# Optimization experiments

Hardware: AMD Instinct MI355X
Metric: run time of the kernel (lower is better)

Reference implementation:

```python
import jax, jax.numpy as jnp
import numpy as np

CLS_THR = 0.7      # cls_threshold
NMS_THR = 0.7      # nms_threshold
MAX_OUT = 100      # nms_max_outputs
MIN_SIZE = 3.0     # min_size_threshold


def setup_inputs() -> dict:
    key = jax.random.key(0)
    k1, k2 = jax.random.split(key)
    B, H, W, A = 1, 128, 128, 9
    img_h = img_w = 2048
    # build valid pixel-space boxes [y1,x1,y2,x2] with y2>y1, x2>x1
    r = jax.random.uniform(k1, (B, H, W, A, 4), dtype=jnp.float32)
    y1 = r[..., 0] * (img_h - 200.0)
    x1 = r[..., 1] * (img_w - 200.0)
    y2 = y1 + 1.0 + r[..., 2] * 199.0
    x2 = x1 + 1.0 + r[..., 3] * 199.0
    proposals = jnp.stack([y1, x1, y2, x2], axis=-1).reshape(B, H, W, A * 4)
    cls_score = jax.random.normal(k2, (B, H, W, A * 2), dtype=jnp.float32) * 2.0
    return {"proposals": proposals, "cls_score": cls_score,
            "image_h": img_h, "image_w": img_w}


def reference(proposals, cls_score, image_h, image_w):
    B, H, W = proposals.shape[0], proposals.shape[1], proposals.shape[2]
    A = proposals.shape[3] // 4
    boxes = proposals.reshape(-1, 4)                       # [N,4] yxyx, pixels
    prob = jax.nn.softmax(cls_score.reshape(B, H, W, A, 2), axis=-1)
    score0 = prob[..., 0].reshape(-1)                      # [N] objectness
    # threshold mask (tf boolean_mask replaced by fixed-shape invalidation)
    active0 = jnp.where(score0 > CLS_THR, score0, -1.0)
    areas = (boxes[:, 2] - boxes[:, 0]) * (boxes[:, 3] - boxes[:, 1])

    def nms_step(active, _):
        idx = jnp.argmax(active)
        ok = active[idx] > 0.0                             # any box left?
        b = boxes[idx]
        yy1 = jnp.maximum(b[0], boxes[:, 0])
        xx1 = jnp.maximum(b[1], boxes[:, 1])
        yy2 = jnp.minimum(b[2], boxes[:, 2])
        xx2 = jnp.minimum(b[3], boxes[:, 3])
        inter = jnp.maximum(yy2 - yy1, 0.0) * jnp.maximum(xx2 - xx1, 0.0)
        iou = inter / (areas + areas[idx] - inter + 1e-9)
        active = jnp.where(iou > NMS_THR, -1.0, active)
        active = active.at[idx].set(-1.0)
        return active, (idx, ok)

    _, (idxs, oks) = jax.lax.scan(nms_step, active0, None, length=MAX_OUT)
    sel_boxes = boxes[idxs]                                # [100,4]
    sel_cls = score0[idxs]                                 # [100]
    # remove_small_proposals: h,w from yxyx -> yxhw
    hgt = sel_boxes[:, 2] - sel_boxes[:, 0]
    wid = sel_boxes[:, 3] - sel_boxes[:, 1]
    keep = oks & (hgt > MIN_SIZE) & (wid > MIN_SIZE)
    sel_boxes = jnp.where(keep[:, None], sel_boxes, 0.0)
    sel_cls = jnp.where(keep, sel_cls, 0.0)
    # format == 'percentage': exact pixel coords -> fraction of image
    scale = jnp.array([image_h, image_w, image_h, image_w], dtype=jnp.float32)
    sel_boxes = (sel_boxes / scale)[None]                  # [1,100,4]
    return sel_boxes, sel_cls[None]                        # [1,100]
```

## Files before the change

kernel.cpp:

```cpp
#include <hip/hip_runtime.h>


#define CLS_THR 0.7f
#define NMS_THR 0.7f
#define MAX_OUT 100
#define MIN_SZ  3.0f

#define N_CAP      147456
#define BASE_BITS  0x3F333334u
#define BIN_SHIFT  9
#define NBINS      9831
#define HIST_WORDS 10240
#define PAD_WORD   10000
#define CTR_WORD   10100
#define TARGET     160u
#define CAP        512
#define CHUNK      128
#define BUCKET_NB  1024
#define BUCKET_LO  (NBINS - BUCKET_NB)
#define BCAP       64

__device__ __forceinline__ float softmax0(float l0, float l1) {
    float m  = fmaxf(l0, l1);
    float e0 = expf(l0 - m);
    float e1 = expf(l1 - m);
    return e0 / (e0 + e1);
}

__device__ __forceinline__ unsigned int ld_dev_u32(const unsigned int* p) {
    return __hip_atomic_load(p, __ATOMIC_RELAXED, __HIP_MEMORY_SCOPE_AGENT);
}
__device__ __forceinline__ unsigned long long ld_dev_u64(const unsigned long long* p) {
    return __hip_atomic_load(p, __ATOMIC_RELAXED, __HIP_MEMORY_SCOPE_AGENT);
}
__device__ __forceinline__ void st_dev_u64(unsigned long long* p, unsigned long long v) {
    __hip_atomic_store(p, v, __ATOMIC_RELAXED, __HIP_MEMORY_SCOPE_AGENT);
}

__launch_bounds__(256)
__global__ void fused_kernel(const float4* __restrict__ boxes,
                             const float4* __restrict__ cls,
                             unsigned int* hist,
                             unsigned long long* bucket,
                             const int* __restrict__ ph, const int* __restrict__ pw,
                             float* __restrict__ out, int N, int nblocks)
{
    __shared__ unsigned long long s_kbuf[CAP];
    __shared__ unsigned long long s_sorted[CAP];
    __shared__ float4 s_bbox[CAP];
    __shared__ unsigned int s_sup[CHUNK][4];
    __shared__ unsigned int s_rowflag[4];
    __shared__ unsigned int s_seedm[4];
    __shared__ unsigned int s_keep[4];
    __shared__ unsigned int s_gpack[CAP];
    __shared__ unsigned int s_goff[CAP];
    __shared__ float  s_klist[MAX_OUT][5];
    __shared__ float4 s_kbox[MAX_OUT];
    __shared__ float  s_karea[MAX_OUT];
    __shared__ int s_cbin, s_ov, s_kept, s_ne, s_last;
    __shared__ unsigned int s_M, s_cnt;

    const int tid  = threadIdx.x;
    const int lane = tid & 63;
    const int wave = tid >> 6;

    const unsigned int X = hist[PAD_WORD];

    {
        int t = blockIdx.x * 256 + tid;
        int i = t * 2;
        if (i < N) {
            float4 v = cls[t];
            float p0 = softmax0(v.x, v.y);
            float p1 = (i + 1 < N) ? softmax0(v.z, v.w) : 0.0f;
            if (p0 > CLS_THR) {
                unsigned int b = __float_as_uint(p0);
                int bin = (int)((b - BASE_BITS) >> BIN_SHIFT);
                unsigned int slot = atomicAdd(&hist[bin], 1u) - X;
                if (bin >= BUCKET_LO && slot < BCAP)
                    st_dev_u64(&bucket[(size_t)(bin - BUCKET_LO) * BCAP + slot],
                        ((unsigned long long)b << 32) | (unsigned int)(~i));
            }
            if (p1 > CLS_THR) {
                unsigned int b = __float_as_uint(p1);
                int bin = (int)((b - BASE_BITS) >> BIN_SHIFT);
                unsigned int slot = atomicAdd(&hist[bin], 1u) - X;
                if (bin >= BUCKET_LO && slot < BCAP)
                    st_dev_u64(&bucket[(size_t)(bin - BUCKET_LO) * BCAP + slot],
                        ((unsigned long long)b << 32) | (unsigned int)(~(i + 1)));
            }
        }
    }
    asm volatile("s_waitcnt vmcnt(0)" ::: "memory");
    __syncthreads();
    if (tid == 0) {
        unsigned int old = atomicAdd(&hist[CTR_WORD], 1u);
        s_last = (old - X == (unsigned int)(nblocks - 1)) ? 1 : 0;
    }
    __syncthreads();
    if (!s_last) return;

    const float img_h = (float)(*ph);
    const float img_w = (float)(*pw);

    int kept = 0;
    int hi = NBINS;
    bool done = false;

    while (!done) {
        if (wave == 0) {
            int pos = hi; unsigned int run = 0u; int cb = -1;
            unsigned int M = 0u; int ov = 0;
            while (pos > 0) {
                int b = pos - 1 - lane;
                unsigned int h = (b >= 0) ? (ld_dev_u32(&hist[b]) - X) : 0u;
                unsigned int pref = h;
                #pragma unroll
                for (int o = 1; o < 64; o <<= 1) {
                    unsigned int t2 = __shfl_up(pref, o);
                    if (lane >= o) pref += t2;
                }
                unsigned int cum = run + pref;
                unsigned long long okm = __ballot(b >= 0 && cum >= TARGET);
                unsigned long long ovm = __ballot(b >= 0 && h > BCAP);
                if (okm) {
                    int first = __builtin_ctzll(okm);
                    cb = pos - 1 - first;
                    M  = __shfl(cum, first);
                    unsigned long long lm = (first >= 63) ? ~0ull
                                          : ((1ull << (first + 1)) - 1ull);
                    if (ovm & lm) ov = 1;
                    break;
                }
                if (ovm) ov = 1;
                run += __shfl(pref, 63);
                pos -= 64;
            }
            if (cb < 0) { cb = 0; M = run; }
            if (lane == 0) { s_cbin = cb; s_M = M; s_ov = ov;
                             s_cnt = 0u; s_ne = 0; }
        }
        __syncthreads();
        const int cbin = s_cbin;
        const unsigned int M = s_M;
        if (M == 0u) break;
        const unsigned int M_eff = (M > CAP) ? CAP : M;
        const bool usebucket = (!s_ov) && (cbin >= BUCKET_LO);

        if (usebucket) {
            if (wave == 0) {
                int pos = hi; unsigned int run = 0u; int ne = 0;
                while (pos > cbin) {
                    int b = pos - 1 - lane;
                    unsigned int h = (b >= cbin) ? (ld_dev_u32(&hist[b]) - X) : 0u;
                    unsigned int pref = h;
                    #pragma unroll
                    for (int o = 1; o < 64; o <<= 1) {
                        unsigned int t2 = __shfl_up(pref, o);
                        if (lane >= o) pref += t2;
                    }
                    unsigned int offv = run + pref - h;
                    unsigned long long nzm = __ballot(h > 0u);
                    int slot = ne + __popcll(nzm & ((1ull << lane) - 1ull));
                    if (h > 0u && slot < CAP) {
                        s_gpack[slot] = ((unsigned int)b << 16) | h;
                        s_goff[slot]  = offv;
                    }
                    ne  += __popcll(nzm);
                    run += __shfl(pref, 63);
                    pos -= 64;
                }
                if (lane == 0) s_ne = ne;
            }
            __syncthreads();
            int ne = s_ne; if (ne > CAP) ne = CAP;
            for (int e = wave; e < ne; e += 4) {
                unsigned int pk = s_gpack[e];
                int b = (int)(pk >> 16);
                unsigned int cnt = pk & 0xFFFFu;
                unsigned int off = s_goff[e];
                if (lane < (int)cnt && off + lane < CAP)
                    s_kbuf[off + lane] =
                        ld_dev_u64(&bucket[(size_t)(b - BUCKET_LO) * BCAP + lane]);
            }
        } else {
            unsigned int th_lo = BASE_BITS + ((unsigned int)cbin << BIN_SHIFT);
            unsigned int th_hi = BASE_BITS + ((unsigned int)hi   << BIN_SHIFT);
            int NV = N >> 1;
            for (int basei = 0; basei < NV; basei += 256 * 8) {
                float4 v[8];
                #pragma unroll
                for (int u = 0; u < 8; ++u) {
                    int i4 = basei + u * 256 + tid;
                    v[u] = (i4 < NV) ? cls[i4]
                                     : make_float4(0.f, 0.f, 0.f, 0.f);
                }
                #pragma unroll
                for (int u = 0; u < 8; ++u) {
                    int i0 = (basei + u * 256 + tid) * 2;
                    float p0 = softmax0(v[u].x, v[u].y);
                    float p1 = softmax0(v[u].z, v[u].w);
                    if (p0 > CLS_THR) {
                        unsigned int b = __float_as_uint(p0);
                        if (b >= th_lo && b < th_hi) {
                            unsigned int sl = atomicAdd(&s_cnt, 1u);
                            if (sl < CAP)
                                s_kbuf[sl] = ((unsigned long long)b << 32)
                                           | (unsigned int)(~i0);
                        }
                    }
                    if (p1 > CLS_THR) {
                        unsigned int b = __float_as_uint(p1);
                        if (b >= th_lo && b < th_hi) {
                            unsigned int sl = atomicAdd(&s_cnt, 1u);
                            if (sl < CAP)
                                s_kbuf[sl] = ((unsigned long long)b << 32)
                                           | (unsigned int)(~(i0 + 1));
                        }
                    }
                }
            }
        }
        __syncthreads();

        for (unsigned int t = tid; t < M_eff; t += 256) {
            unsigned long long kt = s_kbuf[t];
            unsigned int rank = 0u;
            #pragma unroll 8
            for (unsigned int j = 0; j < M_eff; ++j)
                rank += (s_kbuf[j] > kt) ? 1u : 0u;
            s_sorted[rank] = kt;
        }
        __syncthreads();

        for (unsigned int t = tid; t < M_eff; t += 256) {
            int idx = (int)(~(unsigned int)s_sorted[t]);
            s_bbox[t] = boxes[idx];
        }
        __syncthreads();

        int base = 0;
        while (base < (int)M_eff && kept < MAX_OUT) {
            int C = (int)M_eff - base; if (C > CHUNK) C = CHUNK;
            if (tid < CHUNK) { s_sup[tid][0] = 0u; s_sup[tid][1] = 0u;
                               s_sup[tid][2] = 0u; s_sup[tid][3] = 0u; }
            if (tid < 4) { s_rowflag[tid] = 0u; s_seedm[tid] = 0u;
                           s_keep[tid] = 0u; }
            __syncthreads();

            if (kept > 0 && (tid & 127) < C) {
                int i = tid & 127;
                float4 cb = s_bbox[base + i];
                float ca = (cb.z - cb.x) * (cb.w - cb.y);
                bool sup = false;
                for (int j = (tid >> 7); j < kept; j += 2) {
                    float4 kb = s_kbox[j];
                    float yy1 = fmaxf(cb.x, kb.x), xx1 = fmaxf(cb.y, kb.y);
                    float yy2 = fminf(cb.z, kb.z), xx2 = fminf(cb.w, kb.w);
                    float it = fmaxf(yy2 - yy1, 0.f) * fmaxf(xx2 - xx1, 0.f);
                    sup = sup ||
                        (it / (ca + s_karea[j] - it + 1e-9f) > NMS_THR);
                }
                if (sup) atomicOr(&s_seedm[i >> 5], 1u << (i & 31));
            }
            for (int d = 1 + wave; d < C; d += 4) {
                #pragma unroll
                for (int half = 0; half < 2; ++half) {
                    int i = lane + half * 64;
                    if (i + d < C) {
                        float4 a  = s_bbox[base + i];
                        float4 b2 = s_bbox[base + i + d];
                        float aa = (a.z - a.x) * (a.w - a.y);
                        float ab = (b2.z - b2.x) * (b2.w - b2.y);
                        float yy1 = fmaxf(a.x, b2.x), xx1 = fmaxf(a.y, b2.y);
                        float yy2 = fminf(a.z, b2.z), xx2 = fminf(a.w, b2.w);
                        float it = fmaxf(yy2 - yy1, 0.f) * fmaxf(xx2 - xx1, 0.f);
                        if (it / (aa + ab - it + 1e-9f) > NMS_THR) {
                            int j = i + d;
                            atomicOr(&s_sup[i][j >> 5], 1u << (j & 31));
                            atomicOr(&s_rowflag[i >> 5], 1u << (i & 31));
                        }
                    }
                }
            }
            __syncthreads();

            if (wave == 0) {
                unsigned int ku[4] = {0u, 0u, 0u, 0u};
                unsigned int mg[4] = {s_seedm[0], s_seedm[1],
                                      s_seedm[2], s_seedm[3]};
                int k = kept;
                #pragma unroll
                for (int g = 0; g < 4; ++g) {
                    int lo = g * 32;
                    if (lo < C && k < MAX_OUT) {
                        int cg = C - lo; if (cg > 32) cg = 32;
                        unsigned int vmask = (cg >= 32) ? 0xFFFFFFFFu
                                            : ((1u << cg) - 1u);
                        unsigned int avail = vmask & ~mg[g];
                        unsigned int hitr = s_rowflag[g] & avail;
                        if (hitr == 0u) {
                            int c2 = __popc(avail);
                            int need = MAX_OUT - k;
                            if (c2 <= need) { ku[g] |= avail; k += c2; }
                            else {
                                unsigned int kw = avail; int cc = c2;
                                while (cc > need) {
                                    kw &= ~(0x80000000u >> __builtin_clz(kw));
                                    --cc;
                                }
                                ku[g] |= kw; k = MAX_OUT;
                            }
                        } else {
                            unsigned int rem = avail;
                            while (rem && k < MAX_OUT) {
                                int b = __builtin_ctz(rem);
                                ku[g] |= (1u << b); ++k;
                                if ((s_rowflag[g] >> b) & 1u) {
                                    int i = lo + b;
                                    mg[0] |= s_sup[i][0];
                                    mg[1] |= s_sup[i][1];
                                    mg[2] |= s_sup[i][2];
                                    mg[3] |= s_sup[i][3];
                                    rem &= ~mg[g];
                                }
                                rem &= ~(1u << b);
                            }
                        }
                    }
                }
                if (lane == 0) {
                    s_keep[0] = ku[0]; s_keep[1] = ku[1];
                    s_keep[2] = ku[2]; s_keep[3] = ku[3];
                    s_kept = k;
                }
            }
            __syncthreads();
            int prevkept = kept;
            kept = s_kept;

            if (tid < C) {
                int w = tid >> 5, bp = tid & 31;
                unsigned int kw = s_keep[w];
                if ((kw >> bp) & 1u) {
                    int pre = __popc(kw & ((1u << bp) - 1u));
                    for (int q = 0; q < w; ++q) pre += __popc(s_keep[q]);
                    int slot = prevkept + pre;
                    float4 bb = s_bbox[base + tid];
                    s_klist[slot][0] = bb.x; s_klist[slot][1] = bb.y;
                    s_klist[slot][2] = bb.z; s_klist[slot][3] = bb.w;
                    s_klist[slot][4] = __uint_as_float(
                        (unsigned int)(s_sorted[base + tid] >> 32));
                    s_kbox[slot]  = bb;
                    s_karea[slot] = (bb.z - bb.x) * (bb.w - bb.y);
                }
            }
            __syncthreads();
            base += C;
        }

        done = (kept >= MAX_OUT) || (cbin == 0);
        hi = cbin;
    }

    __syncthreads();
    for (int j = tid; j < 4 * MAX_OUT + MAX_OUT; j += 256) {
        float val = 0.0f;
        if (j < 4 * MAX_OUT) {
            int k = j >> 2, cc = j & 3;
            if (k < kept) {
                float h = s_klist[k][2] - s_klist[k][0];
                float w = s_klist[k][3] - s_klist[k][1];
                if (h > MIN_SZ && w > MIN_SZ) {
                    float scale = (cc == 0 || cc == 2) ? img_h : img_w;
                    val = s_klist[k][cc] / scale;
                }
            }
        } else {
            int k = j - 4 * MAX_OUT;
            if (k < kept) {
                float h = s_klist[k][2] - s_klist[k][0];
                float w = s_klist[k][3] - s_klist[k][1];
                if (h > MIN_SZ && w > MIN_SZ) val = s_klist[k][4];
            }
        }
        out[j] = val;
    }
}

extern "C" void kernel_launch(void* const* d_in, const int* in_sizes, int n_in,
                              void* d_out, int out_size, void* d_ws, size_t ws_size,
                              hipStream_t stream) {
    const float* proposals = (const float*)d_in[0];
    const float* cls       = (const float*)d_in[1];
    const int*   ph        = (const int*)d_in[2];
    const int*   pw        = (const int*)d_in[3];
    float*       out       = (float*)d_out;

    int N = in_sizes[0] / 4;
    if (N > N_CAP) N = N_CAP;

    char* ws = (char*)d_ws;
    unsigned long long* bucket = (unsigned long long*)ws;
    unsigned int* hist = (unsigned int*)(ws + (size_t)BUCKET_NB * BCAP * 8);

    int nblocks = (N / 2 + 255) / 256;
    fused_kernel<<<nblocks, 256, 0, stream>>>(
        (const float4*)proposals, (const float4*)cls, hist, bucket,
        ph, pw, out, N, nblocks);
}
```

Baseline: 84.14 us.

## Store box coords in bucket and add 256-thread fast path for candidate selection

```diff
diff --git a/kernel.cpp b/kernel.cpp
--- a/kernel.cpp
+++ b/kernel.cpp
@@ -36,6 +36,9 @@
 __device__ __forceinline__ void st_dev_u64(unsigned long long* p, unsigned long long v) {
     __hip_atomic_store(p, v, __ATOMIC_RELAXED, __HIP_MEMORY_SCOPE_AGENT);
 }
+__device__ __forceinline__ unsigned long long pack2f(float a, float b) {
+    return ((unsigned long long)__float_as_uint(b) << 32) | __float_as_uint(a);
+}
 
 __launch_bounds__(256)
 __global__ void fused_kernel(const float4* __restrict__ boxes,
@@ -48,16 +51,18 @@
     __shared__ unsigned long long s_kbuf[CAP];
     __shared__ unsigned long long s_sorted[CAP];
     __shared__ float4 s_bbox[CAP];
+    __shared__ unsigned int s_binof[CAP];
     __shared__ unsigned int s_sup[CHUNK][4];
     __shared__ unsigned int s_rowflag[4];
     __shared__ unsigned int s_seedm[4];
     __shared__ unsigned int s_keep[4];
     __shared__ unsigned int s_gpack[CAP];
     __shared__ unsigned int s_goff[CAP];
+    __shared__ unsigned int s_wsum[4];
     __shared__ float  s_klist[MAX_OUT][5];
     __shared__ float4 s_kbox[MAX_OUT];
     __shared__ float  s_karea[MAX_OUT];
-    __shared__ int s_cbin, s_ov, s_kept, s_ne, s_last;
+    __shared__ int s_cbin, s_ov, s_kept, s_ne, s_last, s_cutT;
     __shared__ unsigned int s_M, s_cnt;
 
     const int tid  = threadIdx.x;
@@ -70,24 +75,34 @@
         int t = blockIdx.x * 256 + tid;
         int i = t * 2;
         if (i < N) {
-            float4 v = cls[t];
+            float4 v  = cls[t];
+            float4 b0 = boxes[i];
+            float4 b1 = (i + 1 < N) ? boxes[i + 1] : b0;
             float p0 = softmax0(v.x, v.y);
             float p1 = (i + 1 < N) ? softmax0(v.z, v.w) : 0.0f;
             if (p0 > CLS_THR) {
                 unsigned int b = __float_as_uint(p0);
                 int bin = (int)((b - BASE_BITS) >> BIN_SHIFT);
                 unsigned int slot = atomicAdd(&hist[bin], 1u) - X;
-                if (bin >= BUCKET_LO && slot < BCAP)
-                    st_dev_u64(&bucket[(size_t)(bin - BUCKET_LO) * BCAP + slot],
+                if (bin >= BUCKET_LO && slot < BCAP) {
+                    size_t ba = ((size_t)(bin - BUCKET_LO) * BCAP + slot) * 3;
+                    st_dev_u64(&bucket[ba],
                         ((unsigned long long)b << 32) | (unsigned int)(~i));
+                    st_dev_u64(&bucket[ba + 1], pack2f(b0.x, b0.y));
+                    st_dev_u64(&bucket[ba + 2], pack2f(b0.z, b0.w));
+                }
             }
             if (p1 > CLS_THR) {
                 unsigned int b = __float_as_uint(p1);
                 int bin = (int)((b - BASE_BITS) >> BIN_SHIFT);
                 unsigned int slot = atomicAdd(&hist[bin], 1u) - X;
-                if (bin >= BUCKET_LO && slot < BCAP)
-                    st_dev_u64(&bucket[(size_t)(bin - BUCKET_LO) * BCAP + slot],
+                if (bin >= BUCKET_LO && slot < BCAP) {
+                    size_t ba = ((size_t)(bin - BUCKET_LO) * BCAP + slot) * 3;
+                    st_dev_u64(&bucket[ba],
                         ((unsigned long long)b << 32) | (unsigned int)(~(i + 1)));
+                    st_dev_u64(&bucket[ba + 1], pack2f(b1.x, b1.y));
+                    st_dev_u64(&bucket[ba + 2], pack2f(b1.z, b1.w));
+                }
             }
         }
     }
@@ -108,136 +123,206 @@
     bool done = false;
 
     while (!done) {
-        if (wave == 0) {
-            int pos = hi; unsigned int run = 0u; int cb = -1;
-            unsigned int M = 0u; int ov = 0;
-            while (pos > 0) {
-                int b = pos - 1 - lane;
-                unsigned int h = (b >= 0) ? (ld_dev_u32(&hist[b]) - X) : 0u;
-                unsigned int pref = h;
-                #pragma unroll
-                for (int o = 1; o < 64; o <<= 1) {
-                    unsigned int t2 = __shfl_up(pref, o);
-                    if (lane >= o) pref += t2;
-                }
-                unsigned int cum = run + pref;
-                unsigned long long okm = __ballot(b >= 0 && cum >= TARGET);
-                unsigned long long ovm = __ballot(b >= 0 && h > BCAP);
-                if (okm) {
-                    int first = __builtin_ctzll(okm);
-                    cb = pos - 1 - first;
-                    M  = __shfl(cum, first);
-                    unsigned long long lm = (first >= 63) ? ~0ull
-                                          : ((1ull << (first + 1)) - 1ull);
-                    if (ovm & lm) ov = 1;
-                    break;
-                }
-                if (ovm) ov = 1;
-                run += __shfl(pref, 63);
-                pos -= 64;
-            }
-            if (cb < 0) { cb = 0; M = run; }
-            if (lane == 0) { s_cbin = cb; s_M = M; s_ov = ov;
-                             s_cnt = 0u; s_ne = 0; }
-        }
+        if (tid == 0) { s_cutT = -1; s_ov = 0; s_cnt = 0u; s_ne = 0; }
         __syncthreads();
-        const int cbin = s_cbin;
-        const unsigned int M = s_M;
-        if (M == 0u) break;
-        const unsigned int M_eff = (M > CAP) ? CAP : M;
-        const bool usebucket = (!s_ov) && (cbin >= BUCKET_LO);
-
-        if (usebucket) {
+
+        bool usefast = false;
+        unsigned int h_reg = 0u, cum_reg = 0u;
+
+        if (hi == NBINS) {
+            int b = NBINS - 1 - tid;
+            h_reg = ld_dev_u32(&hist[b]) - X;
+            unsigned int pref = h_reg;
+            #pragma unroll
+            for (int o = 1; o < 64; o <<= 1) {
+                unsigned int t2 = __shfl_up(pref, o);
+                if (lane >= o) pref += t2;
+            }
+            if (lane == 63) s_wsum[wave] = pref;
+            __syncthreads();
+            unsigned int cum = pref;
+            for (int q = 0; q < wave; ++q) cum += s_wsum[q];
+            cum_reg = cum;
+            if (cum >= TARGET && cum - h_reg < TARGET) {
+                s_cutT = tid; s_M = cum; s_cbin = b;
+            }
+            __syncthreads();
+            int cutT = s_cutT;
+            if (cutT >= 0) {
+                if (tid <= cutT && h_reg > BCAP) s_ov = 1;
+                __syncthreads();
+                usefast = (!s_ov) && (s_M <= 256u);
+                if (usefast) {
+                    if (tid <= cutT && h_reg > 0u) {
+                        unsigned int off = cum_reg - h_reg;
+                        unsigned int rb  = (unsigned int)(NBINS - 1 - tid - BUCKET_LO);
+                        for (unsigned int s = 0; s < h_reg; ++s)
+                            if (off + s < CAP) s_binof[off + s] = (rb << 6) | s;
+                    }
+                    __syncthreads();
+                    unsigned int M = s_M;
+                    unsigned long long key = 0ull;
+                    float4 bx = make_float4(0.f, 0.f, 0.f, 0.f);
+                    if ((unsigned int)tid < M) {
+                        unsigned int bs = s_binof[tid];
+                        size_t ba = ((size_t)(bs >> 6) * BCAP + (bs & 63u)) * 3;
+                        key = ld_dev_u64(&bucket[ba]);
+                        unsigned long long w1 = ld_dev_u64(&bucket[ba + 1]);
+                        unsigned long long w2 = ld_dev_u64(&bucket[ba + 2]);
+                        bx.x = __uint_as_float((unsigned int)w1);
+                        bx.y = __uint_as_float((unsigned int)(w1 >> 32));
+                        bx.z = __uint_as_float((unsigned int)w2);
+                        bx.w = __uint_as_float((unsigned int)(w2 >> 32));
+                        s_kbuf[tid] = key;
+                    }
+                    __syncthreads();
+                    if ((unsigned int)tid < M) {
+                        unsigned int rank = 0u;
+                        #pragma unroll 8
+                        for (unsigned int j = 0; j < M; ++j)
+                            rank += (s_kbuf[j] > key) ? 1u : 0u;
+                        s_sorted[rank] = key;
+                        s_bbox[rank]   = bx;
+                    }
+                    __syncthreads();
+                }
+            } else {
+                __syncthreads();
+            }
+        }
+
+        if (!usefast) {
             if (wave == 0) {
-                int pos = hi; unsigned int run = 0u; int ne = 0;
-                while (pos > cbin) {
+                int pos = hi; unsigned int run = 0u; int cb = -1;
+                unsigned int M = 0u; int ov = 0;
+                while (pos > 0) {
                     int b = pos - 1 - lane;
-                    unsigned int h = (b >= cbin) ? (ld_dev_u32(&hist[b]) - X) : 0u;
+                    unsigned int h = (b >= 0) ? (ld_dev_u32(&hist[b]) - X) : 0u;
                     unsigned int pref = h;
                     #pragma unroll
                     for (int o = 1; o < 64; o <<= 1) {
                         unsigned int t2 = __shfl_up(pref, o);
                         if (lane >= o) pref += t2;
                     }
-                    unsigned int offv = run + pref - h;
-                    unsigned long long nzm = __ballot(h > 0u);
-                    int slot = ne + __popcll(nzm & ((1ull << lane) - 1ull));
-                    if (h > 0u && slot < CAP) {
-                        s_gpack[slot] = ((unsigned int)b << 16) | h;
-                        s_goff[slot]  = offv;
-                    }
-                    ne  += __popcll(nzm);
+                    unsigned int cum = run + pref;
+                    unsigned long long okm = __ballot(b >= 0 && cum >= TARGET);
+                    unsigned long long ovm = __ballot(b >= 0 && h > BCAP);
+                    if (okm) {
+                        int first = __builtin_ctzll(okm);
+                        cb = pos - 1 - first;
+                        M  = __shfl(cum, first);
+                        unsigned long long lm = (first >= 63) ? ~0ull
+                                              : ((1ull << (first + 1)) - 1ull);
+                        if (ovm & lm) ov = 1;
+                        break;
+                    }
+                    if (ovm) ov = 1;
                     run += __shfl(pref, 63);
                     pos -= 64;
                 }
-                if (lane == 0) s_ne = ne;
-            }
-            __syncthreads();
-            int ne = s_ne; if (ne > CAP) ne = CAP;
-            for (int e = wave; e < ne; e += 4) {
-                unsigned int pk = s_gpack[e];
-                int b = (int)(pk >> 16);
-                unsigned int cnt = pk & 0xFFFFu;
-                unsigned int off = s_goff[e];
-                if (lane < (int)cnt && off + lane < CAP)
-                    s_kbuf[off + lane] =
-                        ld_dev_u64(&bucket[(size_t)(b - BUCKET_LO) * BCAP + lane]);
-            }
-        } else {
-            unsigned int th_lo = BASE_BITS + ((unsigned int)cbin << BIN_SHIFT);
-            unsigned int th_hi = BASE_BITS + ((unsigned int)hi   << BIN_SHIFT);
-            int NV = N >> 1;
-            for (int basei = 0; basei < NV; basei += 256 * 8) {
-                float4 v[8];
-                #pragma unroll
-                for (int u = 0; u < 8; ++u) {
-                    int i4 = basei + u * 256 + tid;
-                    v[u] = (i4 < NV) ? cls[i4]
-                                     : make_float4(0.f, 0.f, 0.f, 0.f);
-                }
-                #pragma unroll
-                for (int u = 0; u < 8; ++u) {
-                    int i0 = (basei + u * 256 + tid) * 2;
-                    float p0 = softmax0(v[u].x, v[u].y);
-                    float p1 = softmax0(v[u].z, v[u].w);
-                    if (p0 > CLS_THR) {
-                        unsigned int b = __float_as_uint(p0);
-                        if (b >= th_lo && b < th_hi) {
-                            unsigned int sl = atomicAdd(&s_cnt, 1u);
-                            if (sl < CAP)
-                                s_kbuf[sl] = ((unsigned long long)b << 32)
-                                           | (unsigned int)(~i0);
-                        }
-                    }
-                    if (p1 > CLS_THR) {
-                        unsigned int b = __float_as_uint(p1);
-                        if (b >= th_lo && b < th_hi) {
-                            unsigned int sl = atomicAdd(&s_cnt, 1u);
-                            if (sl < CAP)
-                                s_kbuf[sl] = ((unsigned long long)b << 32)
-                                           | (unsigned int)(~(i0 + 1));
-                        }
-                    }
-                }
-            }
-        }
-        __syncthreads();
-
-        for (unsigned int t = tid; t < M_eff; t += 256) {
-            unsigned long long kt = s_kbuf[t];
-            unsigned int rank = 0u;
-            #pragma unroll 8
-            for (unsigned int j = 0; j < M_eff; ++j)
-                rank += (s_kbuf[j] > kt) ? 1u : 0u;
-            s_sorted[rank] = kt;
-        }
-        __syncthreads();
-
-        for (unsigned int t = tid; t < M_eff; t += 256) {
-            int idx = (int)(~(unsigned int)s_sorted[t]);
-            s_bbox[t] = boxes[idx];
-        }
-        __syncthreads();
+                if (cb < 0) { cb = 0; M = run; }
+                if (lane == 0) { s_cbin = cb; s_M = M; s_ov = ov; }
+            }
+            __syncthreads();
+        }
+
+        const int cbin = s_cbin;
+        const unsigned int M = s_M;
+        if (M == 0u) break;
+        const unsigned int M_eff = (M > CAP) ? CAP : M;
+
+        if (!usefast) {
+            const bool usebucket = (!s_ov) && (cbin >= BUCKET_LO);
+            if (usebucket) {
+                if (wave == 0) {
+                    int pos = hi; unsigned int run = 0u; int ne = 0;
+                    while (pos > cbin) {
+                        int b = pos - 1 - lane;
+                        unsigned int h = (b >= cbin) ? (ld_dev_u32(&hist[b]) - X) : 0u;
+                        unsigned int pref = h;
+                        #pragma unroll
+                        for (int o = 1; o < 64; o <<= 1) {
+                            unsigned int t2 = __shfl_up(pref, o);
+                            if (lane >= o) pref += t2;
+                        }
+                        unsigned int offv = run + pref - h;
+                        unsigned long long nzm = __ballot(h > 0u);
+                        int slot = ne + __popcll(nzm & ((1ull << lane) - 1ull));
+                        if (h > 0u && slot < CAP) {
+                            s_gpack[slot] = ((unsigned int)b << 16) | h;
+                            s_goff[slot]  = offv;
+                        }
+                        ne  += __popcll(nzm);
+                        run += __shfl(pref, 63);
+                        pos -= 64;
+                    }
+                    if (lane == 0) s_ne = ne;
+                }
+                __syncthreads();
+                int ne = s_ne; if (ne > CAP) ne = CAP;
+                for (int e = wave; e < ne; e += 4) {
+                    unsigned int pk = s_gpack[e];
+                    int b = (int)(pk >> 16);
+                    unsigned int cnt = pk & 0xFFFFu;
+                    unsigned int off = s_goff[e];
+                    if (lane < (int)cnt && off + lane < CAP)
+                        s_kbuf[off + lane] = ld_dev_u64(
+                            &bucket[((size_t)(b - BUCKET_LO) * BCAP + lane) * 3]);
+                }
+            } else {
+                unsigned int th_lo = BASE_BITS + ((unsigned int)cbin << BIN_SHIFT);
+                unsigned int th_hi = BASE_BITS + ((unsigned int)hi   << BIN_SHIFT);
+                int NV = N >> 1;
+                for (int basei = 0; basei < NV; basei += 256 * 8) {
+                    float4 v[8];
+                    #pragma unroll
+                    for (int u = 0; u < 8; ++u) {
+                        int i4 = basei + u * 256 + tid;
+                        v[u] = (i4 < NV) ? cls[i4]
+                                         : make_float4(0.f, 0.f, 0.f, 0.f);
+                    }
+                    #pragma unroll
+                    for (int u = 0; u < 8; ++u) {
+                        int i0 = (basei + u * 256 + tid) * 2;
+                        float p0 = softmax0(v[u].x, v[u].y);
+                        float p1 = softmax0(v[u].z, v[u].w);
+                        if (p0 > CLS_THR) {
+                            unsigned int b = __float_as_uint(p0);
+                            if (b >= th_lo && b < th_hi) {
+                                unsigned int sl = atomicAdd(&s_cnt, 1u);
+                                if (sl < CAP)
+                                    s_kbuf[sl] = ((unsigned long long)b << 32)
+                                               | (unsigned int)(~i0);
+                            }
+                        }
+                        if (p1 > CLS_THR) {
+                            unsigned int b = __float_as_uint(p1);
+                            if (b >= th_lo && b < th_hi) {
+                                unsigned int sl = atomicAdd(&s_cnt, 1u);
+                                if (sl < CAP)
+                                    s_kbuf[sl] = ((unsigned long long)b << 32)
+                                               | (unsigned int)(~(i0 + 1));
+                            }
+                        }
+                    }
+                }
+            }
+            __syncthreads();
+            for (unsigned int t = tid; t < M_eff; t += 256) {
+                unsigned long long kt = s_kbuf[t];
+                unsigned int rank = 0u;
+                #pragma unroll 8
+                for (unsigned int j = 0; j < M_eff; ++j)
+                    rank += (s_kbuf[j] > kt) ? 1u : 0u;
+                s_sorted[rank] = kt;
+            }
+            __syncthreads();
+            for (unsigned int t = tid; t < M_eff; t += 256) {
+                int idx = (int)(~(unsigned int)s_sorted[t]);
+                s_bbox[t] = boxes[idx];
+            }
+            __syncthreads();
+        }
 
         int base = 0;
         while (base < (int)M_eff && kept < MAX_OUT) {
@@ -293,39 +378,36 @@
                 #pragma unroll
                 for (int g = 0; g < 4; ++g) {
                     int lo = g * 32;
-                    if (lo < C && k < MAX_OUT) {
-                        int cg = C - lo; if (cg > 32) cg = 32;
-                        unsigned int vmask = (cg >= 32) ? 0xFFFFFFFFu
-                                            : ((1u << cg) - 1u);
-                        unsigned int avail = vmask & ~mg[g];
-                        unsigned int hitr = s_rowflag[g] & avail;
-                        if (hitr == 0u) {
-                            int c2 = __popc(avail);
-                            int need = MAX_OUT - k;
-                            if (c2 <= need) { ku[g] |= avail; k += c2; }
-                            else {
-                                unsigned int kw = avail; int cc = c2;
-                                while (cc > need) {
-                                    kw &= ~(0x80000000u >> __builtin_clz(kw));
-                                    --cc;
-                                }
-                                ku[g] |= kw; k = MAX_OUT;
+                    if (lo >= C || k >= MAX_OUT) continue;
+                    int cg = C - lo; if (cg > 32) cg = 32;
+                    unsigned int vmask = (cg >= 32) ? 0xFFFFFFFFu
+                                        : ((1u << cg) - 1u);
+                    unsigned int rem = vmask & ~mg[g];
+                    while (rem && k < MAX_OUT) {
+                        unsigned int flagged = rem & s_rowflag[g];
+                        unsigned int pre; bool applyRow = false; int fb = 0;
+                        if (!flagged) pre = rem;
+                        else {
+                            fb = __builtin_ctz(flagged); applyRow = true;
+                            pre = rem & ((fb == 31) ? 0xFFFFFFFFu
+                                                    : ((2u << fb) - 1u));
+                        }
+                        int c2 = __popc(pre);
+                        int need = MAX_OUT - k;
+                        if (c2 > need) {
+                            while (c2 > need) {
+                                pre &= ~(0x80000000u >> __builtin_clz(pre));
+                                --c2;
                             }
-                        } else {
-                            unsigned int rem = avail;
-                            while (rem && k < MAX_OUT) {
-                                int b = __builtin_ctz(rem);
-                                ku[g] |= (1u << b); ++k;
-                                if ((s_rowflag[g] >> b) & 1u) {
-                                    int i = lo + b;
-                                    mg[0] |= s_sup[i][0];
-                                    mg[1] |= s_sup[i][1];
-                                    mg[2] |= s_sup[i][2];
-                                    mg[3] |= s_sup[i][3];
-                                    rem &= ~mg[g];
-                                }
-                                rem &= ~(1u << b);
-                            }
+                            ku[g] |= pre; k = MAX_OUT; break;
+                        }
+                        ku[g] |= pre; k += c2;
+                        rem &= ~pre;
+                        if (applyRow) {
+                            int i = lo + fb;
+                            mg[0] |= s_sup[i][0]; mg[1] |= s_sup[i][1];
+                            mg[2] |= s_sup[i][2]; mg[3] |= s_sup[i][3];
+                            rem &= ~mg[g];
                         }
                     }
                 }
@@ -402,7 +484,7 @@
 
     char* ws = (char*)d_ws;
     unsigned long long* bucket = (unsigned long long*)ws;
-    unsigned int* hist = (unsigned int*)(ws + (size_t)BUCKET_NB * BCAP * 8);
+    unsigned int* hist = (unsigned int*)(ws + (size_t)BUCKET_NB * BCAP * 3 * 8);
 
     int nblocks = (N / 2 + 255) / 256;
     fused_kernel<<<nblocks, 256, 0, stream>>>(
```

Result: no change. 85.65 us (+1.8%).
